# Performance work log

Measured on AMD Instinct MI355X. Metric: run time of the kernel, lower is better.

## Reference

```python
import jax, jax.numpy as jnp
import numpy as np

N, E, H, D, C, L = 20000, 320000, 8, 64, 512, 2  # nodes, edges, heads, head_dim, channels, layers


def layer_norm(x, g, b, eps=1e-5):
    mu = x.mean(-1, keepdims=True)
    var = ((x - mu) ** 2).mean(-1, keepdims=True)
    return (x - mu) / jnp.sqrt(var + eps) * g + b


def setup_inputs() -> dict:
    key = jax.random.key(0)
    ks = jax.random.split(key, 14)
    s = 0.02
    x = jax.random.normal(ks[0], (N, C), jnp.float32)
    edge_index = jax.random.randint(ks[1], (2, E), 0, N, jnp.int32)
    edge_type = jax.random.randint(ks[2], (E,), 0, 10, jnp.int32)
    edge_repre = jax.random.normal(ks[3], (E,), jnp.float32)
    # Per-layer TransformerConv params (query/key/value/skip linears, each with bias)
    Wq = jax.random.normal(ks[4], (L, C, C), jnp.float32) * s
    Wk = jax.random.normal(ks[5], (L, C, C), jnp.float32) * s
    Wv = jax.random.normal(ks[6], (L, C, C), jnp.float32) * s
    Ws = jax.random.normal(ks[7], (L, C, C), jnp.float32) * s
    bq = jnp.zeros((L, C), jnp.float32)
    bk = jnp.zeros((L, C), jnp.float32)
    bv = jnp.zeros((L, C), jnp.float32)
    bs = jnp.zeros((L, C), jnp.float32)
    # FFN + shared LayerNorm
    W1 = jax.random.normal(ks[8], (C, 2 * C), jnp.float32) * s
    b1 = jnp.zeros((2 * C,), jnp.float32)
    W2 = jax.random.normal(ks[9], (2 * C, C), jnp.float32) * s
    b2 = jnp.zeros((C,), jnp.float32)
    ln_g = jnp.ones((C,), jnp.float32)
    ln_b = jnp.zeros((C,), jnp.float32)
    return {"x": x, "edge_index": edge_index, "edge_type": edge_type, "edge_repre": edge_repre,
            "Wq": Wq, "bq": bq, "Wk": Wk, "bk": bk, "Wv": Wv, "bv": bv, "Ws": Ws, "bs": bs,
            "W1": W1, "b1": b1, "W2": W2, "b2": b2, "ln_g": ln_g, "ln_b": ln_b}


def reference(x, edge_index, edge_type, edge_repre, Wq, bq, Wk, bk, Wv, bv, Ws, bs, W1, b1, W2, b2, ln_g, ln_b):
    src, dst = edge_index[0], edge_index[1]  # messages flow src -> dst (PyG source_to_target)
    enc = x
    scale = 1.0 / jnp.sqrt(jnp.float32(D))
    for l in range(L):
        q = (x @ Wq[l] + bq[l]).reshape(N, H, D)
        k = (x @ Wk[l] + bk[l]).reshape(N, H, D)
        v = (x @ Wv[l] + bv[l]).reshape(N, H, D)
        # per-edge attention logits [E, H]
        a = (q[dst] * k[src]).sum(-1) * scale
        # segment softmax over edges sharing a destination node
        amax = jax.ops.segment_max(a, dst, num_segments=N)
        amax = jnp.where(jnp.isfinite(amax), amax, 0.0)
        e = jnp.exp(a - amax[dst])
        denom = jax.ops.segment_sum(e, dst, num_segments=N)
        alpha = e / (denom[dst] + 1e-16)
        # scatter-aggregate weighted values, concat heads
        agg = jax.ops.segment_sum(alpha[:, :, None] * v[src], dst, num_segments=N).reshape(N, C)
        # root/skip connection (beta=False) + module-level residual to enc_emb
        x = agg + (x @ Ws[l] + bs[l]) + enc
    x = layer_norm(x, ln_g, ln_b)
    x = (jax.nn.relu(x @ W1 + b1) @ W2 + b2) + x
    x = layer_norm(x, ln_g, ln_b)
    return x + enc
```

## Files before the change

kernel.cpp:

```cpp
#include <hip/hip_runtime.h>

typedef __attribute__((ext_vector_type(8))) short short8;
typedef __attribute__((ext_vector_type(4))) float f32x4;

__device__ __forceinline__ unsigned short f2b(float f){
  union { float f; unsigned u; } x; x.f = f;
  unsigned r = x.u + 0x7fffu + ((x.u >> 16) & 1u);
  return (unsigned short)(r >> 16);
}
__device__ __forceinline__ float b2f(unsigned short v){
  union { unsigned u; float f; } x; x.u = ((unsigned)v) << 16; return x.f;
}

__device__ __forceinline__ unsigned char enc1(float v){
#if __has_builtin(__builtin_amdgcn_cvt_pk_fp8_f32)
  return (unsigned char)(__builtin_amdgcn_cvt_pk_fp8_f32(v, v, 0, false) & 0xff);
#else
  union{float f;unsigned u;}x; x.f=v;
  unsigned s = x.u >> 31;
  float av = fabsf(v);
  if (av >= 448.f) return (unsigned char)((s<<7)|0x7e);
  if (av < 0.0078125f){ unsigned d=(unsigned)(av*512.f+0.5f); return (unsigned char)((s<<7)|d); }
  unsigned q = x.u & 0x7fffffff;
  q = q + 0x7ffff + ((q>>20)&1);
  int e2 = (int)(q>>23) - 127;
  unsigned m3 = (q>>20)&7;
  if (e2 < -6){ unsigned d=(unsigned)(av*512.f+0.5f); return (unsigned char)((s<<7)|d); }
  return (unsigned char)((s<<7) | ((unsigned)(e2+7)<<3) | m3);
#endif
}
__device__ __forceinline__ unsigned pk4(float a,float b,float c,float d){
#if __has_builtin(__builtin_amdgcn_cvt_pk_fp8_f32)
  int v = __builtin_amdgcn_cvt_pk_fp8_f32(a, b, 0, false);
  v = __builtin_amdgcn_cvt_pk_fp8_f32(c, d, v, true);
  return (unsigned)v;
#else
  return (unsigned)enc1(a) | ((unsigned)enc1(b)<<8) | ((unsigned)enc1(c)<<16) | ((unsigned)enc1(d)<<24);
#endif
}
__device__ __forceinline__ void dec4(unsigned u, float* o){
#if __has_builtin(__builtin_amdgcn_cvt_pk_f32_fp8)
  auto lo = __builtin_amdgcn_cvt_pk_f32_fp8((int)u, false);
  auto hi = __builtin_amdgcn_cvt_pk_f32_fp8((int)u, true);
  o[0]=lo[0]; o[1]=lo[1]; o[2]=hi[0]; o[3]=hi[1];
#else
  #pragma unroll
  for (int j=0;j<4;j++){
    unsigned b = (u >> (8*j)) & 0xffu;
    unsigned s = b >> 7, ex = (b >> 3) & 15u, mn = b & 7u;
    union{unsigned u;float f;} x;
    x.u = ex ? ((s<<31)|((ex+120u)<<23)|(mn<<20)) : (s<<31);
    o[j] = x.f;
  }
#endif
}

__global__ void count_k(const int* __restrict__ dst, int* __restrict__ deg, int E){
  int e = blockIdx.x*256 + threadIdx.x;
  if (e < E) atomicAdd(&deg[dst[e]], 1);
}

__global__ void scan_k(const int* __restrict__ deg, int* __restrict__ rowstart,
                       int* __restrict__ cursor, int n)
{
  __shared__ int wsum[16];
  int tid = threadIdx.x, lane = tid & 63, wv = tid >> 6;
  int CH = (n + 1023) >> 10;
  int b0 = tid * CH; if (b0 > n) b0 = n;
  int bend = b0 + CH; if (bend > n) bend = n;
  int sum = 0;
  for (int i = b0; i < bend; ++i) sum += deg[i];
  int xs = sum;
  #pragma unroll
  for (int o=1;o<64;o<<=1){ int t = __shfl_up(xs, o, 64); if (lane >= o) xs += t; }
  if (lane == 63) wsum[wv] = xs;
  __syncthreads();
  if (tid < 16){
    int w = wsum[tid];
    #pragma unroll
    for (int o=1;o<16;o<<=1){ int t = __shfl_up(w, o, 64); if (tid >= o) w += t; }
    wsum[tid] = w;
  }
  __syncthreads();
  int off = (wv ? wsum[wv-1] : 0) + xs - sum;
  int run = off;
  for (int i = b0; i < bend; ++i){ rowstart[i] = run; cursor[i] = run; run += deg[i]; }
  if (b0 < n && bend == n) rowstart[n] = run;
  if (n == 0 && tid == 0) rowstart[0] = 0;
}

__global__ void fill_k(const int* __restrict__ src, const int* __restrict__ dst,
                       int* __restrict__ cursor, int* __restrict__ csrc, int E){
  int e = blockIdx.x*256 + threadIdx.x;
  if (e < E){
    int p = atomicAdd(&cursor[dst[e]], 1);
    csrc[p] = src[e];
  }
}

__global__ void transpose_all_k(const float* __restrict__ Wq, const float* __restrict__ Wk,
  const float* __restrict__ Wv, const float* __restrict__ Ws,
  const float* __restrict__ W1, const float* __restrict__ W2,
  unsigned char* __restrict__ wtqkvs8, unsigned char* __restrict__ wt1_8,
  unsigned char* __restrict__ wt2_8)
{
  int bid = blockIdx.x;
  const float* src; unsigned char* dst; int r, c, lb;
  if (bid < 1024){
    int j = bid >> 7;
    int l = j >> 2, w = j & 3;
    src = (w==0?Wq : w==1?Wk : w==2?Wv : Ws) + (size_t)l*512*512;
    dst = wtqkvs8 + ((size_t)l*2048 + (size_t)w*512)*512;
    r = 512; c = 512; lb = bid & 127;
  } else if (bid < 1280){ src = W1; dst = wt1_8; r = 512; c = 1024; lb = bid - 1024; }
  else { src = W2; dst = wt2_8; r = 1024; c = 512; lb = bid - 1280; }
  int idx = lb*256 + threadIdx.x;
  int o = idx % c;
  int i0 = (idx / c) << 3;
  float v[8];
  #pragma unroll
  for (int t=0;t<8;t++) v[t] = 64.f * src[(size_t)(i0+t)*c + o];
  unsigned lo = pk4(v[0],v[1],v[2],v[3]);
  unsigned hi = pk4(v[4],v[5],v[6],v[7]);
  *(unsigned long long*)&dst[(size_t)o*r + i0] =
      (unsigned long long)lo | ((unsigned long long)hi << 32);
}

__global__ void cvt8_k(const float* __restrict__ in, unsigned char* __restrict__ out8,
                       unsigned short* __restrict__ outb, size_t n){
  size_t i = ((size_t)blockIdx.x*256 + threadIdx.x)*8;
  if (i >= n) return;
  const float4* p = (const float4*)(in + i);
  float4 a0 = p[0], a1 = p[1];
  short8 vv;
  ((unsigned short*)&vv)[0] = f2b(a0.x); ((unsigned short*)&vv)[1] = f2b(a0.y);
  ((unsigned short*)&vv)[2] = f2b(a0.z); ((unsigned short*)&vv)[3] = f2b(a0.w);
  ((unsigned short*)&vv)[4] = f2b(a1.x); ((unsigned short*)&vv)[5] = f2b(a1.y);
  ((unsigned short*)&vv)[6] = f2b(a1.z); ((unsigned short*)&vv)[7] = f2b(a1.w);
  *(short8*)&outb[i] = vv;
  unsigned lo = pk4(a0.x,a0.y,a0.z,a0.w);
  unsigned hi = pk4(a1.x,a1.y,a1.z,a1.w);
  *(unsigned long long*)&out8[i] = (unsigned long long)lo | ((unsigned long long)hi<<32);
}

template<int MODE, int KC, int NN>
__global__ __launch_bounds__(256) void gemm8_k(
    const unsigned char* __restrict__ A8,
    const unsigned char* __restrict__ Bt8,
    int M,
    const float* __restrict__ bias0, const float* __restrict__ bias1,
    const float* __restrict__ bias2, const float* __restrict__ bias3,
    unsigned short* __restrict__ qb, unsigned short* __restrict__ skipb,
    unsigned char* __restrict__ outC,
    float* __restrict__ outF, const float* __restrict__ res)
{
  __shared__ unsigned char lA[128*128];
  __shared__ unsigned char lB[128*128];
  const int tid  = threadIdx.x;
  const int lane = tid & 63;
  const int wid  = tid >> 6;

  const int nwg = gridDim.x;
  int id = blockIdx.x;
  int q = nwg >> 3, r = nwg & 7;
  int xc = id & 7, yy = id >> 3;
  int swz = (xc < r ? xc*(q+1) : r*(q+1) + (xc-r)*q) + yy;
  const int bm = (swz / NN) * 128;
  const int bn = (swz % NN) * 128;
  const int wm = (wid >> 1) * 64;
  const int wn = (wid & 1) * 64;

  f32x4 acc[4][4];
  #pragma unroll
  for (int m=0;m<4;m++)
    #pragma unroll
    for (int n=0;n<4;n++) acc[m][n] = (f32x4)0.f;

  const int kq  = lane >> 4;
  const int ofs = (kq & 1) * 8;
  const int ch2 = kq >> 1;

  for (int kt = 0; kt < KC; kt += 128){
    #pragma unroll
    for (int it = 0; it < 4; ++it) {
      int chunk = it*256 + tid;
      int row = chunk >> 3;
      int cin = chunk & 7;
      int scol = (cin ^ (row & 7)) * 16;
      int ga = bm + row; if (ga >= M) ga = M - 1;
      __builtin_amdgcn_global_load_lds(
        (const __attribute__((address_space(1))) void*)(A8 + (size_t)ga*KC + kt + scol),
        (__attribute__((address_space(3))) void*)(&lA[(it*256 + (wid<<6))*16]),
        16, 0, 0);
      __builtin_amdgcn_global_load_lds(
        (const __attribute__((address_space(1))) void*)(Bt8 + (size_t)(bn + row)*KC + kt + scol),
        (__attribute__((address_space(3))) void*)(&lB[(it*256 + (wid<<6))*16]),
        16, 0, 0);
    }
    __syncthreads();
    #pragma unroll
    for (int s = 0; s < 4; ++s){
      unsigned long long af[4], bfr[4];
      #pragma unroll
      for (int m=0;m<4;m++){
        int rr = wm + m*16 + (lane & 15);
        int c  = (s*2 + ch2) ^ (rr & 7);
        af[m] = *(const unsigned long long*)&lA[rr*128 + c*16 + ofs];
      }
      #pragma unroll
      for (int n=0;n<4;n++){
        int rr = wn + n*16 + (lane & 15);
        int c  = (s*2 + ch2) ^ (rr & 7);
        bfr[n] = *(const unsigned long long*)&lB[rr*128 + c*16 + ofs];
      }
      #pragma unroll
      for (int m=0;m<4;m++)
        #pragma unroll
        for (int n=0;n<4;n++)
          acc[m][n] = __builtin_amdgcn_mfma_f32_16x16x32_fp8_fp8(
              (long)af[m], (long)bfr[n], acc[m][n], 0,0,0);
    }
    __syncthreads();
  }

  #pragma unroll
  for (int m=0;m<4;m++){
    int row0 = bm + wm + m*16 + ((lane >> 4) << 2);
    #pragma unroll
    for (int n=0;n<4;n++){
      int col = bn + wn + n*16 + (lane & 15);
      float bval;
      if (MODE == 0){
        bval = (col < 512) ? bias0[col]
             : (col < 1024) ? bias1[col-512]
             : (col < 1536) ? bias2[col-1024] : bias3[col-1536];
      } else {
        bval = bias0[col];
      }
      #pragma unroll
      for (int r4=0;r4<4;r4++){
        int row = row0 + r4;
        if (row < M){
          float v = acc[m][n][r4] * 0.015625f + bval;
          if (MODE == 0){
            if (col < 512)       qb[(size_t)row*512 + col] = f2b(v);
            else if (col < 1536) outC[(size_t)row*1024 + (col-512)] = enc1(v);
            else                 skipb[(size_t)row*512 + (col-1536)] = f2b(v);
          } else if (MODE == 1){
            v = fmaxf(v, 0.0f);
            outC[(size_t)row*1024 + col] = enc1(v);
          } else {
            v += res[(size_t)row*512 + col];
            outF[(size_t)row*512 + col] = v;
          }
        }
      }
    }
  }
}

template<int OUT>
__global__ __launch_bounds__(256) void attn_k(
  const unsigned short* __restrict__ qb, const unsigned char* __restrict__ kv8,
  const unsigned short* __restrict__ skipb, const unsigned short* __restrict__ encb,
  const int* __restrict__ rowstart, const int* __restrict__ csrc,
  float* __restrict__ xout, unsigned char* __restrict__ xout8, int N)
{
  int n = blockIdx.x*4 + (threadIdx.x>>6);
  if (n >= N) return;
  int lane = threadIdx.x & 63;
  const short8 qv = *(const short8*)&qb[(size_t)n*512 + lane*8];
  float qf[8];
  #pragma unroll
  for (int j=0;j<8;j++) qf[j] = b2f(((const unsigned short*)&qv)[j]);
  float m = -__builtin_inff(), l = 0.f;
  float acc[8] = {0.f,0.f,0.f,0.f,0.f,0.f,0.f,0.f};
  int e = rowstart[n], e1 = rowstart[n+1];
  if (e < e1){
    int s = csrc[e];
    uint2 kc = *(const uint2*)&kv8[(size_t)s*1024 + lane*8];
    uint2 vc = *(const uint2*)&kv8[(size_t)s*1024 + 512 + lane*8];
    for (; e < e1; ++e){
      int sn = (e+1 < e1) ? csrc[e+1] : s;
      uint2 kn = *(const uint2*)&kv8[(size_t)sn*1024 + lane*8];
      uint2 vn = *(const uint2*)&kv8[(size_t)sn*1024 + 512 + lane*8];
      float kf[8]; dec4(kc.x, kf); dec4(kc.y, kf+4);
      float dot = 0.f;
      #pragma unroll
      for (int j=0;j<8;j++) dot += qf[j]*kf[j];
      dot += __shfl_xor(dot,1); dot += __shfl_xor(dot,2); dot += __shfl_xor(dot,4);
      float a = dot * 0.125f;
      float mn2 = fmaxf(m, a);
      float corr = __expf(m - mn2);
      float p = __expf(a - mn2);
      l = l*corr + p;
      float vf[8]; dec4(vc.x, vf); dec4(vc.y, vf+4);
      #pragma unroll
      for (int j=0;j<8;j++) acc[j] = acc[j]*corr + p*vf[j];
      m = mn2;
      kc = kn; vc = vn;
    }
  }
  float inv = 1.f/(l + 1e-16f);
  size_t base = (size_t)n*512 + (size_t)lane*8;
  const short8 sv = *(const short8*)&skipb[base];
  const short8 ev = *(const short8*)&encb[base];
  float o[8];
  #pragma unroll
  for (int j=0;j<8;j++)
    o[j] = acc[j]*inv + b2f(((const unsigned short*)&sv)[j]) + b2f(((const unsigned short*)&ev)[j]);
  if (OUT == 0){
    unsigned lo = pk4(o[0],o[1],o[2],o[3]);
    unsigned hi = pk4(o[4],o[5],o[6],o[7]);
    *(unsigned long long*)&xout8[base] = (unsigned long long)lo | ((unsigned long long)hi<<32);
  } else {
    float4* po = (float4*)&xout[base];
    po[0] = make_float4(o[0],o[1],o[2],o[3]);
    po[1] = make_float4(o[4],o[5],o[6],o[7]);
  }
}

template<int MODE>
__global__ __launch_bounds__(256) void ln_k(const float* __restrict__ x,
  const float* __restrict__ g, const float* __restrict__ b,
  float* __restrict__ outF, unsigned char* __restrict__ out8,
  const float* __restrict__ addv, int N)
{
  int n = blockIdx.x*4 + (threadIdx.x>>6);
  if (n >= N) return;
  int lane = threadIdx.x & 63;
  size_t base = (size_t)n*512 + (size_t)lane*8;
  const float4* p = (const float4*)(x + base);
  float4 a0 = p[0], a1 = p[1];
  float v[8] = {a0.x,a0.y,a0.z,a0.w,a1.x,a1.y,a1.z,a1.w};
  float s=0.f, ss=0.f;
  #pragma unroll
  for (int j=0;j<8;j++){ s += v[j]; ss += v[j]*v[j]; }
  #pragma unroll
  for (int o=1;o<64;o<<=1){ s += __shfl_xor(s,o); ss += __shfl_xor(ss,o); }
  float mean = s * (1.f/512.f);
  float var  = ss * (1.f/512.f) - mean*mean;
  float rstd = rsqrtf(var + 1e-5f);
  float o[8];
  #pragma unroll
  for (int j=0;j<8;j++){
    int c = lane*8 + j;
    o[j] = (v[j]-mean)*rstd*g[c] + b[c];
  }
  if (MODE == 0){
    float4* po = (float4*)&outF[base];
    po[0] = make_float4(o[0],o[1],o[2],o[3]);
    po[1] = make_float4(o[4],o[5],o[6],o[7]);
    unsigned lo = pk4(o[0],o[1],o[2],o[3]);
    unsigned hi = pk4(o[4],o[5],o[6],o[7]);
    *(unsigned long long*)&out8[base] = (unsigned long long)lo | ((unsigned long long)hi<<32);
  } else {
    #pragma unroll
    for (int j=0;j<8;j++) outF[base+j] = o[j] + addv[base+j];
  }
}

extern "C" void kernel_launch(void* const* d_in, const int* in_sizes, int n_in,
                              void* d_out, int out_size, void* d_ws, size_t ws_size,
                              hipStream_t stream)
{
  const float* x0  = (const float*)d_in[0];
  const int*  eidx = (const int*)d_in[1];
  const float* Wq  = (const float*)d_in[4];
  const float* bq  = (const float*)d_in[5];
  const float* Wk  = (const float*)d_in[6];
  const float* bk  = (const float*)d_in[7];
  const float* Wv  = (const float*)d_in[8];
  const float* bv  = (const float*)d_in[9];
  const float* Wsk = (const float*)d_in[10];
  const float* bs  = (const float*)d_in[11];
  const float* W1  = (const float*)d_in[12];
  const float* b1  = (const float*)d_in[13];
  const float* W2  = (const float*)d_in[14];
  const float* b2  = (const float*)d_in[15];
  const float* lng = (const float*)d_in[16];
  const float* lnb = (const float*)d_in[17];

  const int N = in_sizes[0] / 512;
  const int E = in_sizes[1] / 2;
  const int* esrc = eidx;
  const int* edst = eidx + E;

  char* ws = (char*)d_ws;
  size_t off = 0;
  auto alloc = [&](size_t bytes)->char*{
    char* p = ws + off; off = (off + bytes + 255) & ~(size_t)255; return p;
  };
  unsigned char*  wtqkvs8 = (unsigned char*)alloc((size_t)2*2048*512);
  unsigned char*  wt1_8   = (unsigned char*)alloc((size_t)1024*512);
  unsigned char*  wt2_8   = (unsigned char*)alloc((size_t)512*1024);
  unsigned short* qb      = (unsigned short*)alloc((size_t)N*512*2);
  unsigned char*  kv8     = (unsigned char*)alloc((size_t)N*1024);
  float*          skip    = (float*)alloc((size_t)N*512*4);
  float*          xbuf    = (float*)alloc((size_t)N*512*4);
  unsigned char*  xb8     = (unsigned char*)alloc((size_t)N*512);
  unsigned short* encb    = (unsigned short*)alloc((size_t)N*512*2);
  unsigned short* skipb   = (unsigned short*)alloc((size_t)N*512*2);
  int* deg      = (int*)alloc((size_t)N*4);
  int* rowstart = (int*)alloc((size_t)(N+1)*4);
  int* cursor   = (int*)alloc((size_t)N*4);
  int* csrc     = (int*)alloc((size_t)E*4);
  unsigned char* t8 = (unsigned char*)qb;
  unsigned char* h8 = xb8;

  hipMemsetAsync(deg, 0, (size_t)N*4, stream);
  count_k<<<(E+255)/256, 256, 0, stream>>>(edst, deg, E);
  scan_k<<<1, 1024, 0, stream>>>(deg, rowstart, cursor, N);
  fill_k<<<(E+255)/256, 256, 0, stream>>>(esrc, edst, cursor, csrc, E);

  transpose_all_k<<<1536, 256, 0, stream>>>(Wq, Wk, Wv, Wsk, W1, W2, wtqkvs8, wt1_8, wt2_8);

  const int cvtBlocks = (int)(((size_t)N*512/8 + 255)/256);
  const int rowBlocks = (N + 3)/4;
  const int MB = (N + 127)/128;

  cvt8_k<<<cvtBlocks, 256, 0, stream>>>(x0, xb8, encb, (size_t)N*512);
  for (int l = 0; l < 2; ++l){
    gemm8_k<0,512,16><<<MB*16, 256, 0, stream>>>(xb8, wtqkvs8 + (size_t)l*2048*512, N,
        bq + l*512, bk + l*512, bv + l*512, bs + l*512, qb, skipb, kv8, nullptr, nullptr);
    if (l == 0)
      attn_k<0><<<rowBlocks, 256, 0, stream>>>(qb, kv8, skipb, encb, rowstart, csrc, nullptr, xb8, N);
    else
      attn_k<1><<<rowBlocks, 256, 0, stream>>>(qb, kv8, skipb, encb, rowstart, csrc, xbuf, nullptr, N);
  }

  ln_k<0><<<rowBlocks, 256, 0, stream>>>(xbuf, lng, lnb, skip, h8, nullptr, N);
  gemm8_k<1,512,8><<<MB*8, 256, 0, stream>>>(h8, wt1_8, N,
      b1, nullptr, nullptr, nullptr, nullptr, nullptr, t8, nullptr, nullptr);
  gemm8_k<2,1024,4><<<MB*4, 256, 0, stream>>>(t8, wt2_8, N,
      b2, nullptr, nullptr, nullptr, nullptr, nullptr, nullptr, xbuf, skip);
  ln_k<1><<<rowBlocks, 256, 0, stream>>>(xbuf, lng, lnb, (float*)d_out, nullptr, x0, N);
}
```

Before: 472.3 us.

## Permute FP8 K-slot layout so GEMM fragments load as 16-byte LDS reads

Every producer of FP8 GEMM operands (weight transpose, input convert, attention output, LayerNorm output, FFN1 epilogue) now writes 8-byte K-chunks in a permuted slot order. The GEMM inner loop can then fetch two MFMA k-steps' worth of A/B data with one 128-bit LDS read per row and issue two MFMAs per load. The aim is to halve the number of LDS read instructions in the FP8 GEMMs. The permutation has to match across all producers and consumers, since any inconsistency would silently corrupt results. The FFN1 epilogue also now does scattered byte writes.

```diff
diff --git a/kernel.cpp b/kernel.cpp
--- a/kernel.cpp
+++ b/kernel.cpp
@@ -10,6 +10,10 @@
 }
 __device__ __forceinline__ float b2f(unsigned short v){
   union { unsigned u; float f; } x; x.u = ((unsigned)v) << 16; return x.f;
+}
+
+__device__ __forceinline__ int pslot(int t){
+  return (t & ~7) | ((t & 3) << 1) | ((t >> 2) & 1);
 }
 
 __device__ __forceinline__ unsigned char enc1(float v){
@@ -122,7 +126,7 @@
   for (int t=0;t<8;t++) v[t] = 64.f * src[(size_t)(i0+t)*c + o];
   unsigned lo = pk4(v[0],v[1],v[2],v[3]);
   unsigned hi = pk4(v[4],v[5],v[6],v[7]);
-  *(unsigned long long*)&dst[(size_t)o*r + i0] =
+  *(unsigned long long*)&dst[(size_t)o*r + pslot(i0>>3)*8] =
       (unsigned long long)lo | ((unsigned long long)hi << 32);
 }
 
@@ -140,7 +144,8 @@
   *(short8*)&outb[i] = vv;
   unsigned lo = pk4(a0.x,a0.y,a0.z,a0.w);
   unsigned hi = pk4(a1.x,a1.y,a1.z,a1.w);
-  *(unsigned long long*)&out8[i] = (unsigned long long)lo | ((unsigned long long)hi<<32);
+  size_t op = (i & ~(size_t)511) | ((size_t)pslot((int)((i & 511) >> 3)) << 3);
+  *(unsigned long long*)&out8[op] = (unsigned long long)lo | ((unsigned long long)hi<<32);
 }
 
 template<int MODE, int KC, int NN>
@@ -154,8 +159,8 @@
     unsigned char* __restrict__ outC,
     float* __restrict__ outF, const float* __restrict__ res)
 {
-  __shared__ unsigned char lA[128*128];
-  __shared__ unsigned char lB[128*128];
+  __shared__ __align__(16) unsigned char lA[128*128];
+  __shared__ __align__(16) unsigned char lB[128*128];
   const int tid  = threadIdx.x;
   const int lane = tid & 63;
   const int wid  = tid >> 6;
@@ -176,9 +181,7 @@
     #pragma unroll
     for (int n=0;n<4;n++) acc[m][n] = (f32x4)0.f;
 
-  const int kq  = lane >> 4;
-  const int ofs = (kq & 1) * 8;
-  const int ch2 = kq >> 1;
+  const int kq = lane >> 4;
 
   for (int kt = 0; kt < KC; kt += 128){
     #pragma unroll
@@ -199,26 +202,29 @@
     }
     __syncthreads();
     #pragma unroll
-    for (int s = 0; s < 4; ++s){
-      unsigned long long af[4], bfr[4];
+    for (int S = 0; S < 2; ++S){
+      ulonglong2 af[4], bfv[4];
       #pragma unroll
       for (int m=0;m<4;m++){
         int rr = wm + m*16 + (lane & 15);
-        int c  = (s*2 + ch2) ^ (rr & 7);
-        af[m] = *(const unsigned long long*)&lA[rr*128 + c*16 + ofs];
+        int c  = (S*4 + kq) ^ (rr & 7);
+        af[m] = *(const ulonglong2*)&lA[rr*128 + c*16];
       }
       #pragma unroll
       for (int n=0;n<4;n++){
         int rr = wn + n*16 + (lane & 15);
-        int c  = (s*2 + ch2) ^ (rr & 7);
-        bfr[n] = *(const unsigned long long*)&lB[rr*128 + c*16 + ofs];
+        int c  = (S*4 + kq) ^ (rr & 7);
+        bfv[n] = *(const ulonglong2*)&lB[rr*128 + c*16];
       }
       #pragma unroll
       for (int m=0;m<4;m++)
         #pragma unroll
-        for (int n=0;n<4;n++)
+        for (int n=0;n<4;n++){
           acc[m][n] = __builtin_amdgcn_mfma_f32_16x16x32_fp8_fp8(
-              (long)af[m], (long)bfr[n], acc[m][n], 0,0,0);
+              (long)af[m].x, (long)bfv[n].x, acc[m][n], 0,0,0);
+          acc[m][n] = __builtin_amdgcn_mfma_f32_16x16x32_fp8_fp8(
+              (long)af[m].y, (long)bfv[n].y, acc[m][n], 0,0,0);
+        }
     }
     __syncthreads();
   }
@@ -248,7 +254,9 @@
             else                 skipb[(size_t)row*512 + (col-1536)] = f2b(v);
           } else if (MODE == 1){
             v = fmaxf(v, 0.0f);
-            outC[(size_t)row*1024 + col] = enc1(v);
+            int pc = (col & ~7) | 0;
+            pc = (pslot(col >> 3) << 3) | (col & 7);
+            outC[(size_t)row*1024 + pc] = enc1(v);
           } else {
             v += res[(size_t)row*512 + col];
             outF[(size_t)row*512 + col] = v;
@@ -312,7 +320,8 @@
   if (OUT == 0){
     unsigned lo = pk4(o[0],o[1],o[2],o[3]);
     unsigned hi = pk4(o[4],o[5],o[6],o[7]);
-    *(unsigned long long*)&xout8[base] = (unsigned long long)lo | ((unsigned long long)hi<<32);
+    size_t op = (size_t)n*512 + ((size_t)pslot(lane) << 3);
+    *(unsigned long long*)&xout8[op] = (unsigned long long)lo | ((unsigned long long)hi<<32);
   } else {
     float4* po = (float4*)&xout[base];
     po[0] = make_float4(o[0],o[1],o[2],o[3]);
@@ -353,7 +362,8 @@
     po[1] = make_float4(o[4],o[5],o[6],o[7]);
     unsigned lo = pk4(o[0],o[1],o[2],o[3]);
     unsigned hi = pk4(o[4],o[5],o[6],o[7]);
-    *(unsigned long long*)&out8[base] = (unsigned long long)lo | ((unsigned long long)hi<<32);
+    size_t op = (size_t)n*512 + ((size_t)pslot(lane) << 3);
+    *(unsigned long long*)&out8[op] = (unsigned long long)lo | ((unsigned long long)hi<<32);
   } else {
     #pragma unroll
     for (int j=0;j<8;j++) outF[base+j] = o[j] + addv[base+j];
```

Measured after the change: 458.7 us. -2.9%, faster.
